# Performance work log

Hardware: AMD Instinct MI355X
Metric: run time of the kernel (lower is better)

## Reference

```python
import jax, jax.numpy as jnp
import numpy as np

FP4_VALUES = jnp.array([0.0, 0.5, 1.0, 1.5, 2.0, 3.0, 4.0, 6.0,
                        -0.0, -0.5, -1.0, -1.5, -2.0, -3.0, -4.0, -6.0], dtype=jnp.float32)
ALPHA = 1.702   # swiglu alpha
LIMIT = 7.0     # swiglu clamp limit
TOP_K = 4       # experts per token
EPS = 1e-5      # rmsnorm eps


def dequant_mxfp4(blocks, scales):
    """blocks: [E, R, G, B] int (uint8 values), scales: [E, R, G] int (E8M0 biased exp).
    Returns decoded weights [E, R, G*2B] fp32. Low nibble -> even cols, high nibble -> odd."""
    lo = FP4_VALUES[blocks & 15]
    hi = FP4_VALUES[(blocks >> 4) & 15]
    vals = jnp.stack([lo, hi], axis=-1).reshape(blocks.shape[:-1] + (-1,))  # [E,R,G,2B]
    w = jnp.ldexp(vals, (scales - 127)[..., None])
    return w.reshape(blocks.shape[:-2] + (-1,))


def rmsnorm(x, w):
    return x * jax.lax.rsqrt(jnp.mean(x * x, axis=-1, keepdims=True) + EPS) * w


def setup_inputs():
    key = jax.random.key(0)
    ks = jax.random.split(key, 10)
    E, H, I, B, S = 32, 1024, 1024, 1, 1024
    GB = 16  # packed bytes per 32-element group
    return {
        "x": jax.random.normal(ks[0], (B, S, H), jnp.float32),
        "norm_w": jnp.ones((H,), jnp.float32),
        "gate_w": jax.random.normal(ks[1], (E, H), jnp.float32) * 0.05,
        "gate_b": jax.random.normal(ks[2], (E,), jnp.float32) * 0.01,
        "mlp1_bias": jax.random.normal(ks[3], (E, 2 * I), jnp.float32) * 0.02,
        "mlp2_bias": jax.random.normal(ks[4], (E, H), jnp.float32) * 0.02,
        "mlp1_blocks": jax.random.randint(ks[5], (E, 2 * I, H // 32, GB), 0, 256, jnp.int32),
        "mlp1_scales": jax.random.randint(ks[6], (E, 2 * I, H // 32), 118, 125, jnp.int32),
        "mlp2_blocks": jax.random.randint(ks[7], (E, H, I // 32, GB), 0, 256, jnp.int32),
        "mlp2_scales": jax.random.randint(ks[8], (E, H, I // 32), 118, 125, jnp.int32),
    }


def reference(x, norm_w, gate_w, gate_b, mlp1_bias, mlp2_bias,
              mlp1_blocks, mlp1_scales, mlp2_blocks, mlp2_scales):
    B, S, H = x.shape
    N = B * S
    E = gate_w.shape[0]

    t = rmsnorm(x, norm_w).reshape(N, H)
    logits = t @ gate_w.T + gate_b                      # [N, E]
    top_vals, top_idx = jax.lax.top_k(logits, TOP_K)     # sorted descending, like torch.topk
    top_w = jax.nn.softmax(top_vals, axis=-1)            # [N, K]
    # dense routing matrix: nonzero only at selected experts (indices unique per token)
    route = jnp.zeros((N, E), x.dtype).at[jnp.arange(N)[:, None], top_idx].add(top_w)

    w1 = dequant_mxfp4(mlp1_blocks, mlp1_scales)         # [E, 2I, H]
    w2 = dequant_mxfp4(mlp2_blocks, mlp2_scales)         # [E, H, I]

    h = jnp.einsum('nh,eih->nei', t, w1) + mlp1_bias[None]  # [N, E, 2I]
    x_glu = jnp.minimum(h[..., 0::2], LIMIT)
    x_lin = jnp.clip(h[..., 1::2], -LIMIT, LIMIT)
    a = x_glu * jax.nn.sigmoid(ALPHA * x_glu) * (x_lin + 1.0)   # [N, E, I]
    y = jnp.einsum('nei,ehi->neh', a, w2) + mlp2_bias[None]      # [N, E, H]
    out = jnp.einsum('neh,ne->nh', y, route)                     # weighted combine
    return x + out.reshape(B, S, H)
```

## Files before the change

kernel.cpp:

```cpp
#include <hip/hip_runtime.h>
#include <hip/hip_bf16.h>
#include <math.h>


#define NE 32
#define HD 1024
#define ID 1024
#define NTOK 1024
#define R1 2048

typedef __attribute__((ext_vector_type(8)))  short bf16x8;
typedef __attribute__((ext_vector_type(16))) float f32x16;

#define TB_OFF   0
#define A_OFF    2097152
#define YB_OFF   10485760
#define CNT_OFF  18874368
#define OFFS_OFF 18874624
#define TOKL_OFF 18874880
#define TIDX_OFF 19005952
#define TWT_OFF  19022336
#define POS_OFF  19038720

__device__ __forceinline__ unsigned f2bf(float f) {
    unsigned u = __float_as_uint(f);
    return (u + 0x7FFFu + ((u >> 16) & 1u)) >> 16;
}
__device__ __forceinline__ float bf2f(unsigned u) {
    return __uint_as_float(u << 16);
}

__device__ __forceinline__ bf16x8 dec8(int4 wv, unsigned dd) {
    unsigned u = __builtin_amdgcn_perm((unsigned)wv.y, (unsigned)wv.x, 0x00000400u);
    unsigned v = __builtin_amdgcn_perm((unsigned)wv.w, (unsigned)wv.z, 0x04000000u);
    unsigned packed = __builtin_amdgcn_perm(v, u, 0x07060100u);
    unsigned selE = packed & 0x07070707u;
    unsigned sE   = packed & 0x08080808u;
    unsigned ph   = packed >> 4;
    unsigned selO = ph & 0x07070707u;
    unsigned sO   = ph & 0x08080808u;
    const unsigned PH_hi = 0x40404040u, PH_lo = 0x3F3F3F14u;
    const unsigned PL_hi = 0xC0804000u, PL_lo = 0xC0800000u;
    unsigned hbE = __builtin_amdgcn_perm(PH_hi, PH_lo, selE) | (sE << 4);
    unsigned lbE = __builtin_amdgcn_perm(PL_hi, PL_lo, selE);
    unsigned hbO = __builtin_amdgcn_perm(PH_hi, PH_lo, selO) | (sO << 4);
    unsigned lbO = __builtin_amdgcn_perm(PL_hi, PL_lo, selO);
    unsigned mE0 = __builtin_amdgcn_perm(hbE, lbE, 0x05010400u);
    unsigned mE1 = __builtin_amdgcn_perm(hbE, lbE, 0x07030602u);
    unsigned mO0 = __builtin_amdgcn_perm(hbO, lbO, 0x05010400u);
    unsigned mO1 = __builtin_amdgcn_perm(hbO, lbO, 0x07030602u);
    unsigned r0 = __builtin_amdgcn_perm(mO0, mE0, 0x05040100u);
    unsigned r1 = __builtin_amdgcn_perm(mO0, mE0, 0x07060302u);
    unsigned r2 = __builtin_amdgcn_perm(mO1, mE1, 0x05040100u);
    unsigned r3 = __builtin_amdgcn_perm(mO1, mE1, 0x07060302u);
    unsigned o0, o1, o2, o3;
    asm("v_pk_add_u16 %0, %1, %2" : "=v"(o0) : "v"(r0), "v"(dd));
    asm("v_pk_add_u16 %0, %1, %2" : "=v"(o1) : "v"(r1), "v"(dd));
    asm("v_pk_add_u16 %0, %1, %2" : "=v"(o2) : "v"(r2), "v"(dd));
    asm("v_pk_add_u16 %0, %1, %2" : "=v"(o3) : "v"(r3), "v"(dd));
    uint4 o; o.x = o0; o.y = o1; o.z = o2; o.w = o3;
    union { uint4 u4; bf16x8 b; } cv; cv.u4 = o;
    return cv.b;
}

__device__ __forceinline__ void gll16(const void* g, void* l) {
    __builtin_amdgcn_global_load_lds(
        (const __attribute__((address_space(1))) unsigned int*)g,
        (__attribute__((address_space(3))) unsigned int*)l, 16, 0, 0);
}

#define SB __builtin_amdgcn_sched_barrier(0)

#define BAR_READDONE { asm volatile("s_waitcnt lgkmcnt(0)" ::: "memory"); SB; \
                       __builtin_amdgcn_s_barrier(); SB; }

__global__ __launch_bounds__(256) void k_gate(
    const float* __restrict__ x, const float* __restrict__ norm_w,
    const float* __restrict__ gate_w, const float* __restrict__ gate_b,
    ushort* __restrict__ t_bf16, int* __restrict__ top_idx, float* __restrict__ top_wt,
    int* __restrict__ counts, int* __restrict__ tok_list, int* __restrict__ pos_of)
{
    int n = blockIdx.x;
    int tid = threadIdx.x;
    __shared__ float tl[HD];
    __shared__ float red[4];
    __shared__ float logits[NE];

    const float4* xv = (const float4*)(x + (size_t)n * HD);
    float4 v = xv[tid];
    float ss = v.x * v.x + v.y * v.y + v.z * v.z + v.w * v.w;
    #pragma unroll
    for (int off = 32; off; off >>= 1) ss += __shfl_down(ss, off);
    if ((tid & 63) == 0) red[tid >> 6] = ss;
    __syncthreads();
    float tot = red[0] + red[1] + red[2] + red[3];
    float rms = rsqrtf(tot * (1.0f / HD) + 1e-5f);

    float4 w = ((const float4*)norm_w)[tid];
    float4 tv;
    tv.x = v.x * rms * w.x; tv.y = v.y * rms * w.y;
    tv.z = v.z * rms * w.z; tv.w = v.w * rms * w.w;
    ushort4 tb;
    tb.x = (ushort)f2bf(tv.x); tb.y = (ushort)f2bf(tv.y);
    tb.z = (ushort)f2bf(tv.z); tb.w = (ushort)f2bf(tv.w);
    ((ushort4*)(t_bf16 + (size_t)n * HD))[tid] = tb;
    ((float4*)tl)[tid] = tv;
    __syncthreads();

    int wv = tid >> 6, lane = tid & 63;
    for (int j = 0; j < 8; j++) {
        int e = wv * 8 + j;
        const float* gw = gate_w + (size_t)e * HD;
        float p = 0.f;
        #pragma unroll
        for (int q = 0; q < 16; q++) { int kk = lane + q * 64; p += tl[kk] * gw[kk]; }
        #pragma unroll
        for (int off = 32; off; off >>= 1) p += __shfl_down(p, off);
        if (lane == 0) logits[e] = p + gate_b[e];
    }
    __syncthreads();

    if (tid == 0) {
        float vals[4]; int idx[4];
        unsigned used = 0;
        #pragma unroll
        for (int kk = 0; kk < 4; kk++) {
            float best = -1e30f; int bi = 0;
            for (int e2 = 0; e2 < NE; e2++) {
                if (used & (1u << e2)) continue;
                if (logits[e2] > best) { best = logits[e2]; bi = e2; }
            }
            used |= 1u << bi; vals[kk] = best; idx[kk] = bi;
        }
        float m = vals[0], s = 0.f, ex[4];
        #pragma unroll
        for (int kk = 0; kk < 4; kk++) { ex[kk] = __expf(vals[kk] - m); s += ex[kk]; }
        float inv = 1.0f / s;
        #pragma unroll
        for (int kk = 0; kk < 4; kk++) {
            top_idx[n * 4 + kk] = idx[kk];
            top_wt[n * 4 + kk] = ex[kk] * inv;
            int slot = atomicAdd(counts + idx[kk], 1);
            tok_list[idx[kk] * NTOK + slot] = n;
            pos_of[n * 4 + kk] = slot;
        }
    }
}

__global__ void k_prefix(const int* __restrict__ counts, int* __restrict__ offsets)
{
    if (threadIdx.x == 0) {
        int s = 0;
        for (int e = 0; e < NE; e++) { offsets[e] = s; s += counts[e]; }
        offsets[NE] = s;
    }
}

#define MLP_ISSUE(buf, kt, S0, S1)                                           \
    {                                                                        \
        _Pragma("unroll")                                                    \
        for (int j_ = 0; j_ < 4; j_++)                                       \
            gll16(pw[j_] + (kt) * 128, &wlds[buf][((j_ << 2) + wu) << 10]);  \
        _Pragma("unroll")                                                    \
        for (int i_ = 0; i_ < 4; i_++)                                       \
            gll16(tpp[i_] + (kt) * 64, &tlds[buf][((wu << 2) + i_) << 10]);  \
        S0 = *(const int2*)(spA + (kt) * 2);                                 \
        S1 = *(const int2*)(spB + (kt) * 2);                                 \
    }

#define MLP_COMPUTE(buf, S0, S1)                                             \
    _Pragma("unroll")                                                        \
    for (int ks = 0; ks < 4; ks++) {                                         \
        int s0_ = ks < 2 ? S0.x : S0.y;                                      \
        int s1_ = ks < 2 ? S1.x : S1.y;                                      \
        unsigned d0_ = (unsigned)((s0_ - 127) << 7) & 0xFFFFu;               \
        unsigned d1_ = (unsigned)((s1_ - 127) << 7) & 0xFFFFu;               \
        d0_ |= d0_ << 16; d1_ |= d1_ << 16;                                  \
        int wb_ = (ks * 32 + kh * 16) ^ swzr;                                \
        bf16x8 wf0 = dec8(*(const int4*)&wlds[buf][(wr * 64 + lr) * 128 + wb_], d0_);      \
        bf16x8 wf1 = dec8(*(const int4*)&wlds[buf][(wr * 64 + 32 + lr) * 128 + wb_], d1_); \
        _Pragma("unroll")                                                    \
        for (int mt = 0; mt < 2; mt++) {                                     \
            if (act[mt]) {                                                   \
                bf16x8 af = *(const bf16x8*)&tlds[buf][ks * 4096 +           \
                               (wt * 2 + mt) * 1024 + kh * 512 + lr * 16];   \
                acc[0][mt] = __builtin_amdgcn_mfma_f32_32x32x16_bf16(af, wf0, acc[0][mt], 0, 0, 0); \
                acc[1][mt] = __builtin_amdgcn_mfma_f32_32x32x16_bf16(af, wf1, acc[1][mt], 0, 0, 0); \
            }                                                                \
        }                                                                    \
    }

#define MLP_KLOOP                                                            \
    MLP_ISSUE(0, 0, scA0, scA1);                                             \
    MLP_ISSUE(1, 1, scB0, scB1);                                             \
    SB;                                                                      \
    asm volatile("s_waitcnt vmcnt(10)" ::: "memory"); SB;                    \
    __builtin_amdgcn_s_barrier(); SB;                                        \
    _Pragma("unroll 1")                                                      \
    for (int kt2 = 0; kt2 < 16; kt2 += 2) {                                  \
        MLP_COMPUTE(0, scA0, scA1);                                          \
        BAR_READDONE;                                                        \
        if (kt2 < 14) {                                                      \
            MLP_ISSUE(0, kt2 + 2, scA0, scA1); SB;                           \
            asm volatile("s_waitcnt vmcnt(10)" ::: "memory");                \
        } else {                                                             \
            asm volatile("s_waitcnt vmcnt(0)" ::: "memory");                 \
        }                                                                    \
        SB; __builtin_amdgcn_s_barrier(); SB;                                \
        MLP_COMPUTE(1, scB0, scB1);                                          \
        BAR_READDONE;                                                        \
        if (kt2 < 14) {                                                      \
            MLP_ISSUE(1, kt2 + 3, scB0, scB1); SB;                           \
            asm volatile("s_waitcnt vmcnt(10)" ::: "memory");                \
            SB; __builtin_amdgcn_s_barrier(); SB;                            \
        }                                                                    \
    }

__global__ __launch_bounds__(256, 2) void k_mlp1(
    const ushort* __restrict__ t_bf16, const int* __restrict__ blocks,
    const int* __restrict__ scales, const float* __restrict__ bias,
    const int* __restrict__ counts, const int* __restrict__ offsets,
    const int* __restrict__ tok_list, ushort* __restrict__ a)
{
    int e = blockIdx.y;
    int cnt = counts[e];
    if (cnt == 0) return;
    int r0 = blockIdx.x * 128;
    int tid = threadIdx.x;
    int l = tid & 63;
    int lr = l & 31, kh = l >> 5;
    int wu = __builtin_amdgcn_readfirstlane(tid >> 6);
    int wr = wu >> 1, wt = wu & 1;
    int base = offsets[e];

    __shared__ char tlds[2][16384];
    __shared__ char wlds[2][16384];

    int rowA = r0 + wr * 64 + lr;
    int rowB = rowA + 32;
    const int* spA = scales + (size_t)(e * R1 + rowA) * 32;
    const int* spB = scales + (size_t)(e * R1 + rowB) * 32;
    float blA = bias[e * R1 + rowA];
    float blB = bias[e * R1 + rowB];
    asm volatile("" :: "v"(blA), "v"(blB));

    int swzr = (lr & 7) << 4;
    int scol = ((l & 7) * 16) ^ (((l >> 3) & 7) << 4);
    const char* pw[4];
    #pragma unroll
    for (int j = 0; j < 4; j++)
        pw[j] = (const char*)blocks +
                (size_t)(e * R1 + r0 + j * 32 + wu * 8 + (l >> 3)) * 2048 + scol;
    int sloc8 = (wu * 2 + kh) * 8;

    for (int c0 = 0; c0 < cnt; c0 += 128) {
        int nt = min(128, cnt - c0);
        bool act[2] = { (wt * 2) * 32 < nt, (wt * 2 + 1) * 32 < nt };
        const ushort* tpp[4];
        #pragma unroll
        for (int i = 0; i < 4; i++) {
            int t = i * 32 + (l & 31);
            int tc = t < nt ? t : nt - 1;
            tpp[i] = t_bf16 + (size_t)tok_list[e * NTOK + c0 + tc] * HD + sloc8;
        }
        asm volatile("s_waitcnt vmcnt(0)" ::: "memory"); SB;

        int2 scA0, scA1, scB0, scB1;
        f32x16 acc[2][2] = {};

        MLP_KLOOP;

        #pragma unroll
        for (int nn = 0; nn < 2; nn++) {
            float bl = nn ? blB : blA;
            int row = nn ? rowB : rowA;
            int pcol = row >> 1;
            #pragma unroll
            for (int mt = 0; mt < 2; mt++) {
                if (act[mt]) {
                    #pragma unroll
                    for (int r = 0; r < 16; r++) {
                        float hv = acc[nn][mt][r] + bl;
                        float other = __shfl_xor(hv, 1, 64);
                        int m = (r & 3) + 8 * (r >> 2) + 4 * kh;
                        int tokg = c0 + (wt * 2 + mt) * 32 + m;
                        if (!(l & 1) && tokg < cnt) {
                            float hg = fminf(hv, 7.0f);
                            float hx = fminf(fmaxf(other, -7.0f), 7.0f);
                            float sig = 1.0f / (1.0f + __expf(-1.702f * hg));
                            float av = hg * sig * (hx + 1.0f);
                            a[(size_t)(base + tokg) * ID + pcol] = (ushort)f2bf(av);
                        }
                    }
                }
            }
        }
    }
}

__global__ __launch_bounds__(256, 2) void k_mlp2(
    const ushort* __restrict__ a, const int* __restrict__ blocks,
    const int* __restrict__ scales, const float* __restrict__ bias,
    const int* __restrict__ counts, const int* __restrict__ offsets,
    ushort* __restrict__ yb)
{
    int e = blockIdx.y;
    int cnt = counts[e];
    if (cnt == 0) return;
    int r0 = blockIdx.x * 128;
    int tid = threadIdx.x;
    int l = tid & 63;
    int lr = l & 31, kh = l >> 5;
    int wu = __builtin_amdgcn_readfirstlane(tid >> 6);
    int wr = wu >> 1, wt = wu & 1;
    int base = offsets[e];

    __shared__ char tlds[2][16384];
    __shared__ char wlds[2][16384];

    int rowA = r0 + wr * 64 + lr;
    int rowB = rowA + 32;
    const int* spA = scales + (size_t)(e * HD + rowA) * 32;
    const int* spB = scales + (size_t)(e * HD + rowB) * 32;
    float blA = bias[e * HD + rowA];
    float blB = bias[e * HD + rowB];
    asm volatile("" :: "v"(blA), "v"(blB));

    int swzr = (lr & 7) << 4;
    int scol = ((l & 7) * 16) ^ (((l >> 3) & 7) << 4);
    const char* pw[4];
    #pragma unroll
    for (int j = 0; j < 4; j++)
        pw[j] = (const char*)blocks +
                (size_t)(e * HD + r0 + j * 32 + wu * 8 + (l >> 3)) * 2048 + scol;
    int sloc8 = (wu * 2 + kh) * 8;

    for (int c0 = 0; c0 < cnt; c0 += 128) {
        int nt = min(128, cnt - c0);
        bool act[2] = { (wt * 2) * 32 < nt, (wt * 2 + 1) * 32 < nt };
        const ushort* tpp[4];
        #pragma unroll
        for (int i = 0; i < 4; i++) {
            int t = i * 32 + (l & 31);
            int tc = t < nt ? t : nt - 1;
            tpp[i] = a + (size_t)(base + c0 + tc) * ID + sloc8;
        }
        asm volatile("s_waitcnt vmcnt(0)" ::: "memory"); SB;

        int2 scA0, scA1, scB0, scB1;
        f32x16 acc[2][2] = {};

        MLP_KLOOP;

        #pragma unroll
        for (int nn = 0; nn < 2; nn++) {
            float bl = nn ? blB : blA;
            int row = nn ? rowB : rowA;
            #pragma unroll
            for (int mt = 0; mt < 2; mt++) {
                if (act[mt]) {
                    #pragma unroll
                    for (int r = 0; r < 16; r++) {
                        int m = (r & 3) + 8 * (r >> 2) + 4 * kh;
                        int tokg = c0 + (wt * 2 + mt) * 32 + m;
                        if (tokg < cnt) {
                            float y = acc[nn][mt][r] + bl;
                            yb[(size_t)(base + tokg) * HD + row] = (ushort)f2bf(y);
                        }
                    }
                }
            }
        }
    }
}

__global__ __launch_bounds__(256) void k_combine(
    const float* __restrict__ x, const ushort* __restrict__ yb,
    const int* __restrict__ top_idx, const float* __restrict__ top_wt,
    const int* __restrict__ pos_of, const int* __restrict__ offsets,
    float* __restrict__ out)
{
    int n = blockIdx.x, tid = threadIdx.x;
    float4 xv = ((const float4*)(x + (size_t)n * HD))[tid];
    float r0 = xv.x, r1 = xv.y, r2 = xv.z, r3 = xv.w;
    #pragma unroll
    for (int k = 0; k < 4; k++) {
        int e = top_idx[n * 4 + k];
        float wt = top_wt[n * 4 + k];
        int slot = offsets[e] + pos_of[n * 4 + k];
        ushort4 yv = ((const ushort4*)(yb + (size_t)slot * HD))[tid];
        r0 += wt * bf2f(yv.x); r1 += wt * bf2f(yv.y);
        r2 += wt * bf2f(yv.z); r3 += wt * bf2f(yv.w);
    }
    float4 ov; ov.x = r0; ov.y = r1; ov.z = r2; ov.w = r3;
    ((float4*)(out + (size_t)n * HD))[tid] = ov;
}

extern "C" void kernel_launch(void* const* d_in, const int* in_sizes, int n_in,
                              void* d_out, int out_size, void* d_ws, size_t ws_size,
                              hipStream_t stream)
{
    const float* x           = (const float*)d_in[0];
    const float* norm_w      = (const float*)d_in[1];
    const float* gate_w      = (const float*)d_in[2];
    const float* gate_b      = (const float*)d_in[3];
    const float* mlp1_bias   = (const float*)d_in[4];
    const float* mlp2_bias   = (const float*)d_in[5];
    const int*   mlp1_blocks = (const int*)d_in[6];
    const int*   mlp1_scales = (const int*)d_in[7];
    const int*   mlp2_blocks = (const int*)d_in[8];
    const int*   mlp2_scales = (const int*)d_in[9];
    float* out = (float*)d_out;

    char* ws = (char*)d_ws;
    ushort* t_bf16  = (ushort*)(ws + TB_OFF);
    ushort* a       = (ushort*)(ws + A_OFF);
    ushort* yb      = (ushort*)(ws + YB_OFF);
    int*   counts   = (int*)(ws + CNT_OFF);
    int*   offsets  = (int*)(ws + OFFS_OFF);
    int*   tok_list = (int*)(ws + TOKL_OFF);
    int*   top_idx  = (int*)(ws + TIDX_OFF);
    float* top_wt   = (float*)(ws + TWT_OFF);
    int*   pos_of   = (int*)(ws + POS_OFF);

    hipMemsetAsync(counts, 0, NE * sizeof(int), stream);
    k_gate<<<NTOK, 256, 0, stream>>>(x, norm_w, gate_w, gate_b, t_bf16, top_idx, top_wt,
                                     counts, tok_list, pos_of);
    k_prefix<<<1, 64, 0, stream>>>(counts, offsets);
    k_mlp1<<<dim3(16, NE), 256, 0, stream>>>(t_bf16, mlp1_blocks, mlp1_scales, mlp1_bias,
                                             counts, offsets, tok_list, a);
    k_mlp2<<<dim3(8, NE), 256, 0, stream>>>(a, mlp2_blocks, mlp2_scales, mlp2_bias,
                                            counts, offsets, yb);
    k_combine<<<NTOK, 256, 0, stream>>>(x, yb, top_idx, top_wt, pos_of, offsets, out);
}
```

Before: 192.2 us.

## Repack MXFP4 weights and scales into compact K-tiled layouts before MLP kernels

Adds per-call repack kernels that compress the int32-per-byte weight blocks into packed 4-bit words in a swizzled, K-tile-major layout. They also pack the scale pairs into 16-bit values. The MLP kernels then stream only 4 bytes per row per k-step, with smaller weight LDS buffers. Activations are stored K-chunk-major, occupancy is raised to 3 blocks per SM, and token chunks are split across a new grid z dimension. The repack still reads the full int32 weight arrays on every call, adding extra passes and launches in exchange for lighter, better-coalesced MLP inner loops.

```diff
diff --git a/kernel.cpp b/kernel.cpp
--- a/kernel.cpp
+++ b/kernel.cpp
@@ -12,15 +12,19 @@
 typedef __attribute__((ext_vector_type(8)))  short bf16x8;
 typedef __attribute__((ext_vector_type(16))) float f32x16;
 
-#define TB_OFF   0
-#define A_OFF    2097152
-#define YB_OFF   10485760
-#define CNT_OFF  18874368
-#define OFFS_OFF 18874624
-#define TOKL_OFF 18874880
-#define TIDX_OFF 19005952
-#define TWT_OFF  19022336
-#define POS_OFF  19038720
+#define WP1_OFF  0
+#define YB_OFF   0
+#define WP2_OFF  33554432
+#define SCT1_OFF 50331648
+#define SCT2_OFF 52428800
+#define TK_OFF   53477376
+#define AK_OFF   55574528
+#define CNT_OFF  63963136
+#define OFFS_OFF 63963392
+#define TOKL_OFF 63963648
+#define TIDX_OFF 64094720
+#define TWT_OFF  64111104
+#define POS_OFF  64127488
 
 __device__ __forceinline__ unsigned f2bf(float f) {
     unsigned u = __float_as_uint(f);
@@ -30,10 +34,7 @@
     return __uint_as_float(u << 16);
 }
 
-__device__ __forceinline__ bf16x8 dec8(int4 wv, unsigned dd) {
-    unsigned u = __builtin_amdgcn_perm((unsigned)wv.y, (unsigned)wv.x, 0x00000400u);
-    unsigned v = __builtin_amdgcn_perm((unsigned)wv.w, (unsigned)wv.z, 0x04000000u);
-    unsigned packed = __builtin_amdgcn_perm(v, u, 0x07060100u);
+__device__ __forceinline__ bf16x8 dec8p(unsigned packed, unsigned dd) {
     unsigned selE = packed & 0x07070707u;
     unsigned sE   = packed & 0x08080808u;
     unsigned ph   = packed >> 4;
@@ -70,14 +71,56 @@
 }
 
 #define SB __builtin_amdgcn_sched_barrier(0)
-
 #define BAR_READDONE { asm volatile("s_waitcnt lgkmcnt(0)" ::: "memory"); SB; \
                        __builtin_amdgcn_s_barrier(); SB; }
+
+__global__ __launch_bounds__(256) void k_repack_w(const int* __restrict__ blocks,
+                                                  unsigned* __restrict__ wp, int R)
+{
+    int idx = blockIdx.x * 256 + threadIdx.x;
+    int row = idx & (R - 1);
+    int ekt = idx / R;
+    int e = ekt >> 4, kt = ekt & 15;
+    const int4* src = (const int4*)(blocks + (size_t)(e * R + row) * 512 + kt * 32);
+    unsigned d[8];
+    #pragma unroll
+    for (int q = 0; q < 8; q++) {
+        int4 v = src[q];
+        unsigned u = __builtin_amdgcn_perm((unsigned)v.y, (unsigned)v.x, 0x00000400u);
+        unsigned w = __builtin_amdgcn_perm((unsigned)v.w, (unsigned)v.z, 0x04000000u);
+        d[q] = __builtin_amdgcn_perm(w, u, 0x07060100u);
+    }
+    int x = (row >> 2) & 7;
+    unsigned t;
+    if (x & 1) { t=d[0];d[0]=d[1];d[1]=t; t=d[2];d[2]=d[3];d[3]=t;
+                 t=d[4];d[4]=d[5];d[5]=t; t=d[6];d[6]=d[7];d[7]=t; }
+    if (x & 2) { t=d[0];d[0]=d[2];d[2]=t; t=d[1];d[1]=d[3];d[3]=t;
+                 t=d[4];d[4]=d[6];d[6]=t; t=d[5];d[5]=d[7];d[7]=t; }
+    if (x & 4) { t=d[0];d[0]=d[4];d[4]=t; t=d[1];d[1]=d[5];d[5]=t;
+                 t=d[2];d[2]=d[6];d[6]=t; t=d[3];d[3]=d[7];d[7]=t; }
+    uint4 o0; o0.x=d[0]; o0.y=d[1]; o0.z=d[2]; o0.w=d[3];
+    uint4 o1; o1.x=d[4]; o1.y=d[5]; o1.z=d[6]; o1.w=d[7];
+    *(uint4*)(wp + (size_t)idx * 8) = o0;
+    *(uint4*)(wp + (size_t)idx * 8 + 4) = o1;
+}
+
+__global__ __launch_bounds__(256) void k_repack_sc(const int* __restrict__ scales,
+                                                   ushort* __restrict__ sct, int R)
+{
+    int idx = blockIdx.x * 256 + threadIdx.x;
+    int e = idx / R, row = idx & (R - 1);
+    const int* src = scales + (size_t)idx * 32;
+    #pragma unroll
+    for (int kt = 0; kt < 16; kt++) {
+        int s0 = src[2 * kt], s1 = src[2 * kt + 1];
+        sct[(size_t)(e * 16 + kt) * R + row] = (ushort)((s0 & 0xFF) | ((s1 & 0xFF) << 8));
+    }
+}
 
 __global__ __launch_bounds__(256) void k_gate(
     const float* __restrict__ x, const float* __restrict__ norm_w,
     const float* __restrict__ gate_w, const float* __restrict__ gate_b,
-    ushort* __restrict__ t_bf16, int* __restrict__ top_idx, float* __restrict__ top_wt,
+    ushort* __restrict__ t_k, int* __restrict__ top_idx, float* __restrict__ top_wt,
     int* __restrict__ counts, int* __restrict__ tok_list, int* __restrict__ pos_of)
 {
     int n = blockIdx.x;
@@ -103,7 +146,7 @@
     ushort4 tb;
     tb.x = (ushort)f2bf(tv.x); tb.y = (ushort)f2bf(tv.y);
     tb.z = (ushort)f2bf(tv.z); tb.w = (ushort)f2bf(tv.w);
-    ((ushort4*)(t_bf16 + (size_t)n * HD))[tid] = tb;
+    *(ushort4*)&t_k[((size_t)(tid >> 4) * NTOK + n) * 64 + (tid & 15) * 4] = tb;
     ((float4*)tl)[tid] = tv;
     __syncthreads();
 
@@ -158,32 +201,32 @@
 
 #define MLP_ISSUE(buf, kt, S0, S1)                                           \
     {                                                                        \
-        _Pragma("unroll")                                                    \
-        for (int j_ = 0; j_ < 4; j_++)                                       \
-            gll16(pw[j_] + (kt) * 128, &wlds[buf][((j_ << 2) + wu) << 10]);  \
+        gll16(pwW + (size_t)(kt) * WSTEP, &wlds[buf][wu << 10]);             \
         _Pragma("unroll")                                                    \
         for (int i_ = 0; i_ < 4; i_++)                                       \
-            gll16(tpp[i_] + (kt) * 64, &tlds[buf][((wu << 2) + i_) << 10]);  \
-        S0 = *(const int2*)(spA + (kt) * 2);                                 \
-        S1 = *(const int2*)(spB + (kt) * 2);                                 \
+            gll16(tpp[i_] + (size_t)(kt) * TSTEP,                            \
+                  &tlds[buf][((wu << 2) + i_) << 10]);                       \
+        S0 = (int)spA[(size_t)(kt) * RSC];                                   \
+        S1 = (int)spB[(size_t)(kt) * RSC];                                   \
     }
 
 #define MLP_COMPUTE(buf, S0, S1)                                             \
     _Pragma("unroll")                                                        \
     for (int ks = 0; ks < 4; ks++) {                                         \
-        int s0_ = ks < 2 ? S0.x : S0.y;                                      \
-        int s1_ = ks < 2 ? S1.x : S1.y;                                      \
+        int s0_ = ks < 2 ? (S0 & 0xFF) : (S0 >> 8);                          \
+        int s1_ = ks < 2 ? (S1 & 0xFF) : (S1 >> 8);                          \
         unsigned d0_ = (unsigned)((s0_ - 127) << 7) & 0xFFFFu;               \
         unsigned d1_ = (unsigned)((s1_ - 127) << 7) & 0xFFFFu;               \
         d0_ |= d0_ << 16; d1_ |= d1_ << 16;                                  \
-        int wb_ = (ks * 32 + kh * 16) ^ swzr;                                \
-        bf16x8 wf0 = dec8(*(const int4*)&wlds[buf][(wr * 64 + lr) * 128 + wb_], d0_);      \
-        bf16x8 wf1 = dec8(*(const int4*)&wlds[buf][(wr * 64 + 32 + lr) * 128 + wb_], d1_); \
+        int s_ = ks * 2 + kh;                                                \
+        unsigned w0_ = *(const unsigned*)&wlds[buf][(rl0 * 8 + (s_ ^ wsw)) * 4]; \
+        unsigned w1_ = *(const unsigned*)&wlds[buf][(rl1 * 8 + (s_ ^ wsw)) * 4]; \
+        bf16x8 wf0 = dec8p(w0_, d0_);                                        \
+        bf16x8 wf1 = dec8p(w1_, d1_);                                        \
         _Pragma("unroll")                                                    \
         for (int mt = 0; mt < 2; mt++) {                                     \
             if (act[mt]) {                                                   \
-                bf16x8 af = *(const bf16x8*)&tlds[buf][ks * 4096 +           \
-                               (wt * 2 + mt) * 1024 + kh * 512 + lr * 16];   \
+                bf16x8 af = *(const bf16x8*)&tlds[buf][(((wt * 2 + mt) * 32 + lr) << 7) + ((s_ ^ (lr & 7)) << 4)]; \
                 acc[0][mt] = __builtin_amdgcn_mfma_f32_32x32x16_bf16(af, wf0, acc[0][mt], 0, 0, 0); \
                 acc[1][mt] = __builtin_amdgcn_mfma_f32_32x32x16_bf16(af, wf1, acc[1][mt], 0, 0, 0); \
             }                                                                \
@@ -194,7 +237,7 @@
     MLP_ISSUE(0, 0, scA0, scA1);                                             \
     MLP_ISSUE(1, 1, scB0, scB1);                                             \
     SB;                                                                      \
-    asm volatile("s_waitcnt vmcnt(10)" ::: "memory"); SB;                    \
+    asm volatile("s_waitcnt vmcnt(7)" ::: "memory"); SB;                     \
     __builtin_amdgcn_s_barrier(); SB;                                        \
     _Pragma("unroll 1")                                                      \
     for (int kt2 = 0; kt2 < 16; kt2 += 2) {                                  \
@@ -202,7 +245,7 @@
         BAR_READDONE;                                                        \
         if (kt2 < 14) {                                                      \
             MLP_ISSUE(0, kt2 + 2, scA0, scA1); SB;                           \
-            asm volatile("s_waitcnt vmcnt(10)" ::: "memory");                \
+            asm volatile("s_waitcnt vmcnt(7)" ::: "memory");                 \
         } else {                                                             \
             asm volatile("s_waitcnt vmcnt(0)" ::: "memory");                 \
         }                                                                    \
@@ -211,17 +254,20 @@
         BAR_READDONE;                                                        \
         if (kt2 < 14) {                                                      \
             MLP_ISSUE(1, kt2 + 3, scB0, scB1); SB;                           \
-            asm volatile("s_waitcnt vmcnt(10)" ::: "memory");                \
+            asm volatile("s_waitcnt vmcnt(7)" ::: "memory");                 \
             SB; __builtin_amdgcn_s_barrier(); SB;                            \
         }                                                                    \
     }
 
-__global__ __launch_bounds__(256, 2) void k_mlp1(
-    const ushort* __restrict__ t_bf16, const int* __restrict__ blocks,
-    const int* __restrict__ scales, const float* __restrict__ bias,
+__global__ __launch_bounds__(256, 3) void k_mlp1(
+    const ushort* __restrict__ t_k, const unsigned* __restrict__ wp,
+    const ushort* __restrict__ sct, const float* __restrict__ bias,
     const int* __restrict__ counts, const int* __restrict__ offsets,
-    const int* __restrict__ tok_list, ushort* __restrict__ a)
-{
+    const int* __restrict__ tok_list, ushort* __restrict__ a_k)
+{
+    const int WSTEP = R1 * 32;
+    const int TSTEP = NTOK * 128;
+    const int RSC = R1;
     int e = blockIdx.y;
     int cnt = counts[e];
     if (cnt == 0) return;
@@ -234,38 +280,36 @@
     int base = offsets[e];
 
     __shared__ char tlds[2][16384];
-    __shared__ char wlds[2][16384];
-
-    int rowA = r0 + wr * 64 + lr;
-    int rowB = rowA + 32;
-    const int* spA = scales + (size_t)(e * R1 + rowA) * 32;
-    const int* spB = scales + (size_t)(e * R1 + rowB) * 32;
+    __shared__ char wlds[2][4096];
+
+    int wsw = (lr >> 2) & 7;
+    int rl0 = wr * 64 + lr, rl1 = rl0 + 32;
+    int rowA = r0 + rl0, rowB = r0 + rl1;
+    const ushort* spA = sct + (size_t)e * 16 * R1 + rowA;
+    const ushort* spB = spA + 32;
     float blA = bias[e * R1 + rowA];
     float blB = bias[e * R1 + rowB];
     asm volatile("" :: "v"(blA), "v"(blB));
 
-    int swzr = (lr & 7) << 4;
-    int scol = ((l & 7) * 16) ^ (((l >> 3) & 7) << 4);
-    const char* pw[4];
-    #pragma unroll
-    for (int j = 0; j < 4; j++)
-        pw[j] = (const char*)blocks +
-                (size_t)(e * R1 + r0 + j * 32 + wu * 8 + (l >> 3)) * 2048 + scol;
-    int sloc8 = (wu * 2 + kh) * 8;
-
-    for (int c0 = 0; c0 < cnt; c0 += 128) {
+    const char* pwW = (const char*)wp + (size_t)e * 16 * R1 * 32 + (size_t)r0 * 32
+                      + (wu << 10) + (l << 4);
+    int blk = ((l & 7) ^ ((l >> 3) & 7)) << 4;
+    int g0 = r0 >> 7;
+
+    for (int c0 = blockIdx.z * 128; c0 < cnt; c0 += 256) {
         int nt = min(128, cnt - c0);
         bool act[2] = { (wt * 2) * 32 < nt, (wt * 2 + 1) * 32 < nt };
-        const ushort* tpp[4];
+        const char* tpp[4];
         #pragma unroll
         for (int i = 0; i < 4; i++) {
-            int t = i * 32 + (l & 31);
+            int t = wu * 32 + i * 8 + (l >> 3);
             int tc = t < nt ? t : nt - 1;
-            tpp[i] = t_bf16 + (size_t)tok_list[e * NTOK + c0 + tc] * HD + sloc8;
+            int n = tok_list[e * NTOK + c0 + tc];
+            tpp[i] = (const char*)t_k + (size_t)n * 128 + blk;
         }
         asm volatile("s_waitcnt vmcnt(0)" ::: "memory"); SB;
 
-        int2 scA0, scA1, scB0, scB1;
+        int scA0, scA1, scB0, scB1;
         f32x16 acc[2][2] = {};
 
         MLP_KLOOP;
@@ -274,7 +318,7 @@
         for (int nn = 0; nn < 2; nn++) {
             float bl = nn ? blB : blA;
             int row = nn ? rowB : rowA;
-            int pcol = row >> 1;
+            int cc = (row >> 1) & 63;
             #pragma unroll
             for (int mt = 0; mt < 2; mt++) {
                 if (act[mt]) {
@@ -289,7 +333,8 @@
                             float hx = fminf(fmaxf(other, -7.0f), 7.0f);
                             float sig = 1.0f / (1.0f + __expf(-1.702f * hg));
                             float av = hg * sig * (hx + 1.0f);
-                            a[(size_t)(base + tokg) * ID + pcol] = (ushort)f2bf(av);
+                            a_k[(size_t)g0 * 262144 + (size_t)(base + tokg) * 64 + cc]
+                                = (ushort)f2bf(av);
                         }
                     }
                 }
@@ -298,12 +343,15 @@
     }
 }
 
-__global__ __launch_bounds__(256, 2) void k_mlp2(
-    const ushort* __restrict__ a, const int* __restrict__ blocks,
-    const int* __restrict__ scales, const float* __restrict__ bias,
+__global__ __launch_bounds__(256, 3) void k_mlp2(
+    const ushort* __restrict__ a_k, const unsigned* __restrict__ wp,
+    const ushort* __restrict__ sct, const float* __restrict__ bias,
     const int* __restrict__ counts, const int* __restrict__ offsets,
     ushort* __restrict__ yb)
 {
+    const int WSTEP = HD * 32;
+    const int TSTEP = 4096 * 128;
+    const int RSC = HD;
     int e = blockIdx.y;
     int cnt = counts[e];
     if (cnt == 0) return;
@@ -316,38 +364,34 @@
     int base = offsets[e];
 
     __shared__ char tlds[2][16384];
-    __shared__ char wlds[2][16384];
-
-    int rowA = r0 + wr * 64 + lr;
-    int rowB = rowA + 32;
-    const int* spA = scales + (size_t)(e * HD + rowA) * 32;
-    const int* spB = scales + (size_t)(e * HD + rowB) * 32;
+    __shared__ char wlds[2][4096];
+
+    int wsw = (lr >> 2) & 7;
+    int rl0 = wr * 64 + lr, rl1 = rl0 + 32;
+    int rowA = r0 + rl0, rowB = r0 + rl1;
+    const ushort* spA = sct + (size_t)e * 16 * HD + rowA;
+    const ushort* spB = spA + 32;
     float blA = bias[e * HD + rowA];
     float blB = bias[e * HD + rowB];
     asm volatile("" :: "v"(blA), "v"(blB));
 
-    int swzr = (lr & 7) << 4;
-    int scol = ((l & 7) * 16) ^ (((l >> 3) & 7) << 4);
-    const char* pw[4];
-    #pragma unroll
-    for (int j = 0; j < 4; j++)
-        pw[j] = (const char*)blocks +
-                (size_t)(e * HD + r0 + j * 32 + wu * 8 + (l >> 3)) * 2048 + scol;
-    int sloc8 = (wu * 2 + kh) * 8;
-
-    for (int c0 = 0; c0 < cnt; c0 += 128) {
+    const char* pwW = (const char*)wp + (size_t)e * 16 * HD * 32 + (size_t)r0 * 32
+                      + (wu << 10) + (l << 4);
+    int blk = ((l & 7) ^ ((l >> 3) & 7)) << 4;
+
+    for (int c0 = blockIdx.z * 128; c0 < cnt; c0 += 256) {
         int nt = min(128, cnt - c0);
         bool act[2] = { (wt * 2) * 32 < nt, (wt * 2 + 1) * 32 < nt };
-        const ushort* tpp[4];
+        const char* tpp[4];
         #pragma unroll
         for (int i = 0; i < 4; i++) {
-            int t = i * 32 + (l & 31);
+            int t = wu * 32 + i * 8 + (l >> 3);
             int tc = t < nt ? t : nt - 1;
-            tpp[i] = a + (size_t)(base + c0 + tc) * ID + sloc8;
+            tpp[i] = (const char*)a_k + (size_t)(base + c0 + tc) * 128 + blk;
         }
         asm volatile("s_waitcnt vmcnt(0)" ::: "memory"); SB;
 
-        int2 scA0, scA1, scB0, scB1;
+        int scA0, scA1, scB0, scB1;
         f32x16 acc[2][2] = {};
 
         MLP_KLOOP;
@@ -413,8 +457,12 @@
     float* out = (float*)d_out;
 
     char* ws = (char*)d_ws;
-    ushort* t_bf16  = (ushort*)(ws + TB_OFF);
-    ushort* a       = (ushort*)(ws + A_OFF);
+    unsigned* wp1   = (unsigned*)(ws + WP1_OFF);
+    unsigned* wp2   = (unsigned*)(ws + WP2_OFF);
+    ushort* sct1    = (ushort*)(ws + SCT1_OFF);
+    ushort* sct2    = (ushort*)(ws + SCT2_OFF);
+    ushort* t_k     = (ushort*)(ws + TK_OFF);
+    ushort* a_k     = (ushort*)(ws + AK_OFF);
     ushort* yb      = (ushort*)(ws + YB_OFF);
     int*   counts   = (int*)(ws + CNT_OFF);
     int*   offsets  = (int*)(ws + OFFS_OFF);
@@ -424,12 +472,16 @@
     int*   pos_of   = (int*)(ws + POS_OFF);
 
     hipMemsetAsync(counts, 0, NE * sizeof(int), stream);
-    k_gate<<<NTOK, 256, 0, stream>>>(x, norm_w, gate_w, gate_b, t_bf16, top_idx, top_wt,
+    k_repack_w<<<NE * R1 * 16 / 256, 256, 0, stream>>>(mlp1_blocks, wp1, R1);
+    k_repack_w<<<NE * HD * 16 / 256, 256, 0, stream>>>(mlp2_blocks, wp2, HD);
+    k_repack_sc<<<NE * R1 / 256, 256, 0, stream>>>(mlp1_scales, sct1, R1);
+    k_repack_sc<<<NE * HD / 256, 256, 0, stream>>>(mlp2_scales, sct2, HD);
+    k_gate<<<NTOK, 256, 0, stream>>>(x, norm_w, gate_w, gate_b, t_k, top_idx, top_wt,
                                      counts, tok_list, pos_of);
     k_prefix<<<1, 64, 0, stream>>>(counts, offsets);
-    k_mlp1<<<dim3(16, NE), 256, 0, stream>>>(t_bf16, mlp1_blocks, mlp1_scales, mlp1_bias,
-                                             counts, offsets, tok_list, a);
-    k_mlp2<<<dim3(8, NE), 256, 0, stream>>>(a, mlp2_blocks, mlp2_scales, mlp2_bias,
-                                            counts, offsets, yb);
+    k_mlp1<<<dim3(16, NE, 2), 256, 0, stream>>>(t_k, wp1, sct1, mlp1_bias,
+                                                counts, offsets, tok_list, a_k);
+    k_mlp2<<<dim3(8, NE, 2), 256, 0, stream>>>(a_k, wp2, sct2, mlp2_bias,
+                                               counts, offsets, yb);
     k_combine<<<NTOK, 256, 0, stream>>>(x, yb, top_idx, top_wt, pos_of, offsets, out);
 }
```

Result: slower. 198.0 us (+3.1%).
